# Kernel optimization log

Hardware: AMD Instinct MI355X
Metric: run time of the kernel (lower is better)

Reference implementation:

```python
import jax, jax.numpy as jnp
from jax import lax
import numpy as np

B, T, N, C_IN = 32, 24, 2048, 2
HID, EMB, HORIZON, OUT_DIM = 64, 16, 12, 1


def setup_inputs() -> dict:
    key = jax.random.key(0)
    ks = jax.random.split(key, 8)
    s = 0.05
    return {
        "x": jax.random.normal(ks[0], (B, T, N, C_IN), dtype=jnp.float32),
        "E": jax.random.normal(ks[1], (N, EMB), dtype=jnp.float32),
        "W1": jax.random.normal(ks[2], (C_IN + HID, 4 * HID), dtype=jnp.float32) * s,
        "b1": jnp.zeros((4 * HID,), dtype=jnp.float32),
        "W2": jax.random.normal(ks[3], (HID + HID, 4 * HID), dtype=jnp.float32) * s,
        "b2": jnp.zeros((4 * HID,), dtype=jnp.float32),
        "Wp": jax.random.normal(ks[4], (HID, OUT_DIM * HORIZON), dtype=jnp.float32) * s,
        "bp": jnp.zeros((OUT_DIM * HORIZON,), dtype=jnp.float32),
    }


def _cell(A, xt, h, c, W, b):
    # Graph-conv LSTM cell: A @ [x, h] -> 4 gates
    comb = jnp.concatenate([xt, h], axis=-1)            # [B,N,in+H]
    conv = jnp.einsum("nm,bmc->bnc", A, comb)           # adaptive graph conv
    gates = conv @ W + b                                  # [B,N,4H]
    i, f, g, o = jnp.split(gates, 4, axis=-1)
    c_new = jax.nn.sigmoid(f) * c + jax.nn.sigmoid(i) * jnp.tanh(g)
    h_new = jax.nn.sigmoid(o) * jnp.tanh(c_new)
    return h_new, c_new


def reference(x, E, W1, b1, W2, b2, Wp, bp):
    # Adaptive adjacency: softmax(relu(E E^T)) row-normalized
    A = jax.nn.softmax(jax.nn.relu(E @ E.T), axis=1)      # [N,N]
    b, t, n, _ = x.shape
    z = jnp.zeros((b, n, HID), dtype=x.dtype)
    init = ((z, z), (z, z))

    def step(carry, xt):
        (h1, c1), (h2, c2) = carry
        h1, c1 = _cell(A, xt, h1, c1, W1, b1)
        h2, c2 = _cell(A, h1, h2, c2, W2, b2)
        return ((h1, c1), (h2, c2)), None

    carry, _ = lax.scan(step, init, jnp.moveaxis(x, 1, 0))  # scan over T
    h_last = carry[1][0]                                     # [B,N,H]
    out = h_last @ Wp + bp                                   # [B,N,HORIZON*OUT]
    out = out.reshape(b, n, HORIZON, OUT_DIM).transpose(0, 2, 1, 3)
    return out                                               # [B,HORIZON,N,OUT]
```

## Files before the change

kernel.cpp:

```cpp
#include <hip/hip_runtime.h>
#include <hip/hip_bf16.h>
#include <cstddef>
#include <cstdint>

#define NN   2048
#define BB   32
#define TT   24
#define CIN  2
#define HH   64
#define EMBD 16
#define HOR  12
#define XC   (TT*BB*CIN)
#define PW   4096
#define KC   6144
#define NT   96

using bfrag  = __attribute__((ext_vector_type(8))) short;
using f32x4  = __attribute__((ext_vector_type(4))) float;

static __device__ __forceinline__ short f2bf(float f) {
    __hip_bfloat16 h = __float2bfloat16(f);
    return *reinterpret_cast<short*>(&h);
}
static __device__ __forceinline__ float bf2f(short s) {
    __hip_bfloat16 h;
    *reinterpret_cast<short*>(&h) = s;
    return __bfloat162float(h);
}
static __device__ __forceinline__ unsigned int packsplit(float v) {
    short hb = f2bf(v);
    short lb = f2bf(v - bf2f(hb));
    return (unsigned int)(unsigned short)hb | ((unsigned int)(unsigned short)lb << 16);
}

#define AS1 __attribute__((address_space(1)))
#define AS3 __attribute__((address_space(3)))
static __device__ __forceinline__ void gload16(const short* g, short* l) {
    __builtin_amdgcn_global_load_lds((const AS1 void*)g, (AS3 void*)l, 16, 0, 0);
}

__global__ __launch_bounds__(256) void compute_A_kernel(const float* __restrict__ E,
                                                        short* __restrict__ A2) {
    __shared__ float srow[NN];
    __shared__ float sred[256];
    int row = blockIdx.x;
    float er[EMBD];
#pragma unroll
    for (int k = 0; k < EMBD; ++k) er[k] = E[row*EMBD + k];
    float lmax = -1e30f;
    for (int j = threadIdx.x; j < NN; j += 256) {
        const float* ej = E + j*EMBD;
        float d = 0.f;
#pragma unroll
        for (int k = 0; k < EMBD; ++k) d = fmaf(er[k], ej[k], d);
        d = fmaxf(d, 0.f);
        srow[j] = d;
        lmax = fmaxf(lmax, d);
    }
    sred[threadIdx.x] = lmax;
    __syncthreads();
    for (int s = 128; s > 0; s >>= 1) {
        if (threadIdx.x < s) sred[threadIdx.x] = fmaxf(sred[threadIdx.x], sred[threadIdx.x+s]);
        __syncthreads();
    }
    float rmax = sred[0];
    __syncthreads();
    float lsum = 0.f;
    for (int j = threadIdx.x; j < NN; j += 256) {
        float e = expf(srow[j] - rmax);
        srow[j] = e;
        lsum += e;
    }
    sred[threadIdx.x] = lsum;
    __syncthreads();
    for (int s = 128; s > 0; s >>= 1) {
        if (threadIdx.x < s) sred[threadIdx.x] += sred[threadIdx.x+s];
        __syncthreads();
    }
    float rinv = 1.f / sred[0];
    for (int j = threadIdx.x; j < NN; j += 256) {
        float v = srow[j] * rinv;
        short h = f2bf(v);
        short l = f2bf(v - bf2f(h));
        size_t base = (size_t)row*KC + j;
        A2[base]        = h;
        A2[base + 2048] = h;
        A2[base + 4096] = l;
    }
}

__global__ void scatter_xall(const float* __restrict__ x,
                             short* __restrict__ hi, short* __restrict__ lo) {
    int idx = blockIdx.x*256 + threadIdx.x;
    int n = idx & (NN-1);
    int col = idx >> 11;
    int c = col & 1, b = (col >> 1) & 31, t = col >> 6;
    float v = x[(size_t)(((size_t)b*TT + t)*NN + n)*CIN + c];
    short h = f2bf(v);
    size_t o = (size_t)col*NN + n;
    hi[o] = h;
    lo[o] = f2bf(v - bf2f(h));
}

__global__ void wsplit_T(const float* __restrict__ W, int rowoff, int Kd,
                         short* __restrict__ hi, short* __restrict__ lo) {
    int id = blockIdx.x*256 + threadIdx.x;
    if (id >= 256*Kd) return;
    int j = id / Kd, c = id - j*Kd;
    float v = W[(size_t)(rowoff + c)*256 + j];
    short h = f2bf(v);
    hi[id] = h;
    lo[id] = f2bf(v - bf2f(h));
}

__global__ __launch_bounds__(256, 3) void gc3_gemm(
        const short* __restrict__ Ahi, const short* __restrict__ Alo,
        const short* __restrict__ Bhi, const short* __restrict__ Blo,
        float* __restrict__ Cout, int outStride, int astr) {
    __shared__ short As[12288];
    short* AsHi = As;
    short* AsLo = As + 2048;
    short* BsHi = As + 4096;
    short* BsLo = As + 8192;
    const int t = threadIdx.x;
    const int w = t >> 6, lane = t & 63;
    const int wm = w >> 1, wn = w & 1;
    const int fr = lane & 15, fc = lane >> 4;
    const int rowbase = blockIdx.y * 64;
    const int colbase = blockIdx.x * 128;

    const int rp = t >> 3, ql = t & 7;
    const int qs = ql ^ (rp & 7);
    const int srow = rp*2 + (qs >> 2);
    const int sch  = (qs & 3) * 8;
    const short* aHiS = Ahi + (size_t)(rowbase + srow)*astr + sch;
    const short* aLoS = Alo + (size_t)(rowbase + srow)*astr + sch;
    const short* bHiS = Bhi + (size_t)(colbase + srow)*NN + sch;
    const short* bLoS = Blo + (size_t)(colbase + srow)*NN + sch;
    const size_t bHalf = (size_t)64*NN;

    short* aHiD  = AsHi + t*8;
    short* aLoD  = AsLo + t*8;
    short* bHiD0 = BsHi + t*8;
    short* bHiD1 = BsHi + 2048 + t*8;
    short* bLoD0 = BsLo + t*8;
    short* bLoD1 = BsLo + 2048 + t*8;

    auto ldsoff = [](int row, int f) {
        int rr = row >> 1;
        int q = (((row & 1) << 2) | f) ^ (rr & 7);
        return rr*64 + q*8;
    };
    int aoff[2], boff[4];
#pragma unroll
    for (int m = 0; m < 2; ++m) aoff[m] = ldsoff(wm*32 + m*16 + fr, fc);
#pragma unroll
    for (int n = 0; n < 4; ++n) boff[n] = ldsoff(wn*64 + n*16 + fr, fc);

    f32x4 acc[2][4];
#pragma unroll
    for (int m = 0; m < 2; ++m)
#pragma unroll
        for (int n = 0; n < 4; ++n)
#pragma unroll
            for (int r = 0; r < 4; ++r) acc[m][n][r] = 0.f;

    for (int k0 = 0; k0 < NN; k0 += 32) {
        gload16(aHiS, aHiD);
        gload16(aLoS, aLoD);
        gload16(bHiS, bHiD0);
        gload16(bHiS + bHalf, bHiD1);
        gload16(bLoS, bLoD0);
        gload16(bLoS + bHalf, bLoD1);
        aHiS += 32; aLoS += 32; bHiS += 32; bLoS += 32;
        __syncthreads();
        bfrag ah[2], al[2], bh[4], bl[4];
#pragma unroll
        for (int m = 0; m < 2; ++m) {
            ah[m] = *(const bfrag*)(AsHi + aoff[m]);
            al[m] = *(const bfrag*)(AsLo + aoff[m]);
        }
#pragma unroll
        for (int n = 0; n < 4; ++n) {
            bh[n] = *(const bfrag*)(BsHi + boff[n]);
            bl[n] = *(const bfrag*)(BsLo + boff[n]);
        }
#pragma unroll
        for (int m = 0; m < 2; ++m)
#pragma unroll
            for (int n = 0; n < 4; ++n) {
                acc[m][n] = __builtin_amdgcn_mfma_f32_16x16x32_bf16(ah[m], bh[n], acc[m][n], 0, 0, 0);
                acc[m][n] = __builtin_amdgcn_mfma_f32_16x16x32_bf16(ah[m], bl[n], acc[m][n], 0, 0, 0);
                acc[m][n] = __builtin_amdgcn_mfma_f32_16x16x32_bf16(al[m], bh[n], acc[m][n], 0, 0, 0);
            }
        __syncthreads();
    }
#pragma unroll
    for (int m = 0; m < 2; ++m) {
        const int gr = rowbase + wm*32 + m*16 + fc*4;
#pragma unroll
        for (int n = 0; n < 4; ++n) {
            const int gc = colbase + wn*64 + n*16 + fr;
#pragma unroll
            for (int r = 0; r < 4; ++r)
                Cout[(size_t)(gr + r)*outStride + gc] = acc[m][n][r];
        }
    }
}

__global__ __launch_bounds__(512, 2) void gemm8p(
        const short* __restrict__ A2, const short* __restrict__ B2,
        unsigned int* __restrict__ Cpk, int colstart) {
    __shared__ short lds[3*24576];
    const int tid = threadIdx.x;
    const int w = tid >> 6, lane = tid & 63;
    const int wm = w >> 2, wn = w & 3;
    const int fr = lane & 15, fc = lane >> 4;
    const int gx = gridDim.x;
    const int nwg = gx * gridDim.y;
    const int fid = blockIdx.y * gx + blockIdx.x;
    const int swz = (fid & 7) * (nwg >> 3) + (fid >> 3);
    const int rowbase = (swz / gx) * 128;
    const int colbase = colstart + (swz % gx) * 256;

    const int srl = tid >> 3;
    const int sck = (tid & 7) ^ (srl & 7);
    const short* aS0 = A2 + (size_t)(rowbase + srl)*KC + sck*8;
    const short* aS1 = A2 + (size_t)(rowbase + 64 + srl)*KC + sck*8;
    const short* bS0 = B2 + (size_t)(colbase + srl)*KC + sck*8;
    const short* bS1 = B2 + (size_t)(colbase + 64 + srl)*KC + sck*8;
    const short* bS2 = B2 + (size_t)(colbase + 128 + srl)*KC + sck*8;
    const short* bS3 = B2 + (size_t)(colbase + 192 + srl)*KC + sck*8;

    auto sw = [](int row, int chunk) {
        int c2 = chunk ^ (row & 7);
        return row*64 + c2*8;
    };
    int aoff[4][2], boff[4][2];
#pragma unroll
    for (int m = 0; m < 4; ++m)
#pragma unroll
        for (int kk = 0; kk < 2; ++kk)
            aoff[m][kk] = sw(wm*64 + m*16 + fr, kk*4 + fc);
#pragma unroll
    for (int n = 0; n < 4; ++n)
#pragma unroll
        for (int kk = 0; kk < 2; ++kk)
            boff[n][kk] = 8192 + sw(wn*64 + n*16 + fr, kk*4 + fc);

    bfrag a[4][2], b[4][2];
    f32x4 acc[4][4];
#pragma unroll
    for (int m = 0; m < 4; ++m)
#pragma unroll
        for (int n = 0; n < 4; ++n)
#pragma unroll
            for (int r = 0; r < 4; ++r) acc[m][n][r] = 0.f;

    auto MFMA8 = [&](int m0, int n0) {
#pragma unroll
        for (int dm = 0; dm < 2; ++dm)
#pragma unroll
            for (int dn = 0; dn < 2; ++dn)
#pragma unroll
                for (int kk = 0; kk < 2; ++kk)
                    acc[m0+dm][n0+dn] = __builtin_amdgcn_mfma_f32_16x16x32_bf16(
                        a[m0+dm][kk], b[n0+dn][kk], acc[m0+dm][n0+dn], 0, 0, 0);
    };

    short* bC = lds;
    short* bN = lds + 24576;
    short* bP = lds + 49152;

    gload16(aS0, bC + tid*8);            gload16(aS1, bC + 4096 + tid*8);
    gload16(bS0, bC + 8192 + tid*8);     gload16(bS1, bC + 12288 + tid*8);
    gload16(bS2, bC + 16384 + tid*8);    gload16(bS3, bC + 20480 + tid*8);
    gload16(aS0 + 64, bN + tid*8);          gload16(aS1 + 64, bN + 4096 + tid*8);
    gload16(bS0 + 64, bN + 8192 + tid*8);   gload16(bS1 + 64, bN + 12288 + tid*8);
    gload16(bS2 + 64, bN + 16384 + tid*8);  gload16(bS3 + 64, bN + 20480 + tid*8);

    for (int t = 0; t < NT; ++t) {
        if (t < NT-1) { asm volatile("s_waitcnt vmcnt(6)" ::: "memory"); }
        else          { asm volatile("s_waitcnt vmcnt(0)" ::: "memory"); }
        __builtin_amdgcn_s_barrier();
        __builtin_amdgcn_sched_barrier(0);
        const bool pf = (t + 2 < NT);
        const int toff = (t + 2) * 64;
#pragma unroll
        for (int kk = 0; kk < 2; ++kk) {
            a[0][kk] = *(const bfrag*)(bC + aoff[0][kk]);
            a[1][kk] = *(const bfrag*)(bC + aoff[1][kk]);
            b[0][kk] = *(const bfrag*)(bC + boff[0][kk]);
            b[1][kk] = *(const bfrag*)(bC + boff[1][kk]);
        }
        if (pf) {
            gload16(aS0 + toff, bP + tid*8);
            gload16(aS1 + toff, bP + 4096 + tid*8);
        }
        __builtin_amdgcn_s_barrier();
        __builtin_amdgcn_sched_barrier(0);
        __builtin_amdgcn_s_setprio(1);
        MFMA8(0, 0);
        __builtin_amdgcn_s_setprio(0);
        __builtin_amdgcn_s_barrier();
        __builtin_amdgcn_sched_barrier(0);
#pragma unroll
        for (int kk = 0; kk < 2; ++kk) {
            b[2][kk] = *(const bfrag*)(bC + boff[2][kk]);
            b[3][kk] = *(const bfrag*)(bC + boff[3][kk]);
        }
        if (pf) {
            gload16(bS0 + toff, bP + 8192 + tid*8);
            gload16(bS1 + toff, bP + 12288 + tid*8);
        }
        __builtin_amdgcn_s_barrier();
        __builtin_amdgcn_sched_barrier(0);
        __builtin_amdgcn_s_setprio(1);
        MFMA8(0, 2);
        __builtin_amdgcn_s_setprio(0);
        __builtin_amdgcn_s_barrier();
        __builtin_amdgcn_sched_barrier(0);
#pragma unroll
        for (int kk = 0; kk < 2; ++kk) {
            a[2][kk] = *(const bfrag*)(bC + aoff[2][kk]);
            a[3][kk] = *(const bfrag*)(bC + aoff[3][kk]);
        }
        if (pf) {
            gload16(bS2 + toff, bP + 16384 + tid*8);
            gload16(bS3 + toff, bP + 20480 + tid*8);
        }
        __builtin_amdgcn_s_barrier();
        __builtin_amdgcn_sched_barrier(0);
        __builtin_amdgcn_s_setprio(1);
        MFMA8(2, 0);
        __builtin_amdgcn_s_setprio(0);
        __builtin_amdgcn_s_barrier();
        __builtin_amdgcn_sched_barrier(0);
        __builtin_amdgcn_s_setprio(1);
        MFMA8(2, 2);
        __builtin_amdgcn_s_setprio(0);
        short* tmp = bC; bC = bN; bN = bP; bP = tmp;
    }
#pragma unroll
    for (int m = 0; m < 4; ++m) {
        const int gr0 = rowbase + wm*64 + m*16 + fc*4;
#pragma unroll
        for (int n = 0; n < 4; ++n) {
            const int gc = colbase + wn*64 + n*16 + fr;
#pragma unroll
            for (int r = 0; r < 4; ++r)
                Cpk[(size_t)(gr0 + r)*PW + gc] = packsplit(acc[m][n][r]);
        }
    }
}

template<int NCH, bool XEP>
__global__ __launch_bounds__(256, 2) void cell_mfma(
        const unsigned int* __restrict__ P,
        const float* __restrict__ convX,
        const float* __restrict__ Wx,
        const short* __restrict__ Wthi, const short* __restrict__ Wtlo,
        const float* __restrict__ bias,
        float* __restrict__ cbuf,
        short* __restrict__ hout,
        int tstep) {
    const int t = threadIdx.x;
    const int w = t >> 6, lane = t & 63;
    const int fr = lane & 15, fc = lane >> 4;
    const int b = blockIdx.y;
    const int n0blk = blockIdx.x * 128;
    constexpr int KW = NCH*32;

    bfrag bh[4][NCH], bl[4][NCH];
#pragma unroll
    for (int g = 0; g < 4; ++g)
#pragma unroll
        for (int ch = 0; ch < NCH; ++ch) {
            size_t o = (size_t)((g*4 + w)*16 + fr)*KW + ch*32 + fc*8;
            bh[g][ch] = *(const bfrag*)(Wthi + o);
            bl[g][ch] = *(const bfrag*)(Wtlo + o);
        }
    const int k = w*16 + fr;
    float bs[4], wx0[4], wx1[4];
#pragma unroll
    for (int g = 0; g < 4; ++g) {
        bs[g] = bias[g*64 + k];
        if (XEP) { wx0[g] = Wx[g*64 + k]; wx1[g] = Wx[256 + g*64 + k]; }
    }
    int colb[NCH];
#pragma unroll
    for (int ch = 0; ch < NCH; ++ch)
        colb[ch] = (NCH == 2 || ch < 2) ? (2048 + b*64 + ch*32)
                                        : (b*64 + (ch-2)*32);
    const int cc = lane >> 4;
    const size_t crow = (size_t)(b*64 + k)*NN;
    const size_t hrow = (size_t)(b*64 + k)*KC;

    for (int nt = 0; nt < 8; ++nt) {
        const int n0 = n0blk + nt*16;
        bfrag ah[NCH], al[NCH];
#pragma unroll
        for (int ch = 0; ch < NCH; ++ch) {
            const unsigned int* ap = P + (size_t)(n0 + fr)*PW + colb[ch] + fc*8;
            uint4 u0 = *(const uint4*)ap;
            uint4 u1 = *(const uint4*)(ap + 4);
            unsigned int uu[8] = {u0.x,u0.y,u0.z,u0.w,u1.x,u1.y,u1.z,u1.w};
#pragma unroll
            for (int i = 0; i < 8; ++i) {
                ah[ch][i] = (short)(uu[i] & 0xffffu);
                al[ch][i] = (short)(uu[i] >> 16);
            }
        }
        f32x4 acc[4];
#pragma unroll
        for (int g = 0; g < 4; ++g)
#pragma unroll
            for (int r = 0; r < 4; ++r) acc[g][r] = 0.f;
#pragma unroll
        for (int ch = 0; ch < NCH; ++ch)
#pragma unroll
            for (int g = 0; g < 4; ++g) {
                acc[g] = __builtin_amdgcn_mfma_f32_16x16x32_bf16(ah[ch], bh[g][ch], acc[g], 0, 0, 0);
                acc[g] = __builtin_amdgcn_mfma_f32_16x16x32_bf16(ah[ch], bl[g][ch], acc[g], 0, 0, 0);
                acc[g] = __builtin_amdgcn_mfma_f32_16x16x32_bf16(al[ch], bh[g][ch], acc[g], 0, 0, 0);
            }
        const int nb = n0 + cc*4;
        float4 cold = *(const float4*)(cbuf + crow + nb);
        float xa0[4], xa1[4];
        if (XEP) {
#pragma unroll
            for (int r = 0; r < 4; ++r) {
                float2 cx = *(const float2*)(convX + (size_t)(nb + r)*XC + tstep*64 + b*2);
                xa0[r] = cx.x; xa1[r] = cx.y;
            }
        }
        float cn[4], hv[4];
#pragma unroll
        for (int r = 0; r < 4; ++r) {
            float pg[4];
#pragma unroll
            for (int g = 0; g < 4; ++g) {
                pg[g] = acc[g][r] + bs[g];
                if (XEP) pg[g] += xa0[r]*wx0[g] + xa1[r]*wx1[g];
            }
            float gi = 1.f/(1.f + expf(-pg[0]));
            float gf = 1.f/(1.f + expf(-pg[1]));
            float gg = tanhf(pg[2]);
            float go = 1.f/(1.f + expf(-pg[3]));
            float co = (&cold.x)[r];
            cn[r] = gf*co + gi*gg;
            hv[r] = go * tanhf(cn[r]);
        }
        *(float4*)(cbuf + crow + nb) = make_float4(cn[0], cn[1], cn[2], cn[3]);
        short hh[4], hl[4];
#pragma unroll
        for (int r = 0; r < 4; ++r) {
            hh[r] = f2bf(hv[r]);
            hl[r] = f2bf(hv[r] - bf2f(hh[r]));
        }
        short4 h4 = make_short4(hh[0], hh[1], hh[2], hh[3]);
        short4 l4 = make_short4(hl[0], hl[1], hl[2], hl[3]);
        *(short4*)(hout + hrow + nb)        = h4;
        *(short4*)(hout + hrow + 2048 + nb) = l4;
        *(short4*)(hout + hrow + 4096 + nb) = h4;
    }
}

__global__ __launch_bounds__(256) void proj_T(const short* __restrict__ B2,
        const float* __restrict__ Wp, const float* __restrict__ bp,
        float* __restrict__ out) {
    __shared__ float sW[HH*HOR];
    __shared__ float sb[HOR];
    for (int i = threadIdx.x; i < HH*HOR; i += 256) sW[i] = Wp[i];
    if (threadIdx.x < HOR) sb[threadIdx.x] = bp[threadIdx.x];
    __syncthreads();
    int idx = blockIdx.x*256 + threadIdx.x;
    int b = idx >> 11, n = idx & (NN-1);
    float acc[HOR];
#pragma unroll
    for (int j = 0; j < HOR; ++j) acc[j] = sb[j];
    for (int k = 0; k < HH; ++k) {
        size_t row = (size_t)(b*64 + k)*KC + n;
        float h = bf2f(B2[row]) + bf2f(B2[row + 2048]);
#pragma unroll
        for (int j = 0; j < HOR; ++j) acc[j] = fmaf(h, sW[k*HOR + j], acc[j]);
    }
#pragma unroll
    for (int j = 0; j < HOR; ++j)
        out[(size_t)(b*HOR + j)*NN + n] = acc[j];
}

extern "C" void kernel_launch(void* const* d_in, const int* in_sizes, int n_in,
                              void* d_out, int out_size, void* d_ws, size_t ws_size,
                              hipStream_t stream) {
    const float* x  = (const float*)d_in[0];
    const float* E  = (const float*)d_in[1];
    const float* W1 = (const float*)d_in[2];
    const float* b1 = (const float*)d_in[3];
    const float* W2 = (const float*)d_in[4];
    const float* b2 = (const float*)d_in[5];
    const float* Wp = (const float*)d_in[6];
    const float* bp = (const float*)d_in[7];
    float* out = (float*)d_out;

    char* base = (char*)d_ws;
    short* A2     = (short*)base; base += (size_t)NN*KC*2;
    float* convX  = (float*)base; base += (size_t)NN*XC*4;
    unsigned int* P = (unsigned int*)base; base += (size_t)NN*PW*4;
    short* B2     = (short*)base; base += (size_t)PW*KC*2;
    float* cs1    = (float*)base; base += (size_t)NN*NN*4;
    float* cs2    = (float*)base; base += (size_t)NN*NN*4;
    short* Wt2hi  = (short*)base; base += 256*128*2;
    short* Wt2lo  = (short*)base; base += 256*128*2;
    short* Wt1hi  = (short*)base; base += 256*64*2;
    short* Wt1lo  = (short*)base; base += 256*64*2;
    short* XThi = (short*)P;
    short* XTlo = XThi + (size_t)XC*NN;
    short* h2out = B2;
    short* h1out = B2 + (size_t)NN*KC;

    hipMemsetAsync(cs1, 0, (size_t)NN*NN*4, stream);
    hipMemsetAsync(cs2, 0, (size_t)NN*NN*4, stream);

    compute_A_kernel<<<NN, 256, 0, stream>>>(E, A2);
    wsplit_T<<<(256*128 + 255)/256, 256, 0, stream>>>(W2, 0, 128, Wt2hi, Wt2lo);
    wsplit_T<<<(256*64 + 255)/256, 256, 0, stream>>>(W1, 2, 64, Wt1hi, Wt1lo);
    scatter_xall<<<(XC*NN)/256, 256, 0, stream>>>(x, XThi, XTlo);
    gc3_gemm<<<dim3(XC/128, NN/64), 256, 0, stream>>>(
        A2, A2 + 4096, XThi, XTlo, convX, XC, KC);
    hipMemsetAsync(P, 0, (size_t)NN*PW*4, stream);

    cell_mfma<2, true><<<dim3(NN/128, BB), 256, 0, stream>>>(
        P, convX, W1, Wt1hi, Wt1lo, b1, cs1, h1out, 0);
    gemm8p<<<dim3(8, 16), 512, 0, stream>>>(A2, B2, P, 2048);

    for (int t = 0; t < TT; ++t) {
        cell_mfma<4, false><<<dim3(NN/128, BB), 256, 0, stream>>>(
            P, nullptr, nullptr, Wt2hi, Wt2lo, b2, cs2, h2out, 0);
        if (t < TT-1) {
            cell_mfma<2, true><<<dim3(NN/128, BB), 256, 0, stream>>>(
                P, convX, W1, Wt1hi, Wt1lo, b1, cs1, h1out, t+1);
            gemm8p<<<dim3(16, 16), 512, 0, stream>>>(A2, B2, P, 0);
        }
    }
    proj_T<<<(BB*NN)/256, 256, 0, stream>>>(B2, Wp, bp, out);
}
```

Before: 4.148 ms.

## Simplify gemm8p main loop and fuse layer-2/layer-1 cell launches

The gemm8p inner loop drops its four-phase interleave of LDS reads, global prefetches and MFMA groups with many barriers. Instead it issues all prefetches at once, then all fragment loads, then all 32 MFMAs. Separately, the two per-timestep cell kernels (layer-2 update and next-step layer-1 update) are merged into one launch using blockIdx.z to pick which cell a block runs, halving cell launches and letting both run concurrently. The simpler GEMM schedule gives up fine-grained overlap of LDS reads with MFMA and drops barriers that may have been guarding the triple-buffer reuse.

```diff
diff --git a/kernel.cpp b/kernel.cpp
--- a/kernel.cpp
+++ b/kernel.cpp
@@ -257,17 +257,6 @@
 #pragma unroll
             for (int r = 0; r < 4; ++r) acc[m][n][r] = 0.f;
 
-    auto MFMA8 = [&](int m0, int n0) {
-#pragma unroll
-        for (int dm = 0; dm < 2; ++dm)
-#pragma unroll
-            for (int dn = 0; dn < 2; ++dn)
-#pragma unroll
-                for (int kk = 0; kk < 2; ++kk)
-                    acc[m0+dm][n0+dn] = __builtin_amdgcn_mfma_f32_16x16x32_bf16(
-                        a[m0+dm][kk], b[n0+dn][kk], acc[m0+dm][n0+dn], 0, 0, 0);
-    };
-
     short* bC = lds;
     short* bN = lds + 24576;
     short* bP = lds + 49152;
@@ -283,61 +272,32 @@
         if (t < NT-1) { asm volatile("s_waitcnt vmcnt(6)" ::: "memory"); }
         else          { asm volatile("s_waitcnt vmcnt(0)" ::: "memory"); }
         __builtin_amdgcn_s_barrier();
-        __builtin_amdgcn_sched_barrier(0);
-        const bool pf = (t + 2 < NT);
-        const int toff = (t + 2) * 64;
-#pragma unroll
-        for (int kk = 0; kk < 2; ++kk) {
-            a[0][kk] = *(const bfrag*)(bC + aoff[0][kk]);
-            a[1][kk] = *(const bfrag*)(bC + aoff[1][kk]);
-            b[0][kk] = *(const bfrag*)(bC + boff[0][kk]);
-            b[1][kk] = *(const bfrag*)(bC + boff[1][kk]);
-        }
-        if (pf) {
+        if (t + 2 < NT) {
+            const int toff = (t + 2) * 64;
             gload16(aS0 + toff, bP + tid*8);
             gload16(aS1 + toff, bP + 4096 + tid*8);
-        }
-        __builtin_amdgcn_s_barrier();
-        __builtin_amdgcn_sched_barrier(0);
-        __builtin_amdgcn_s_setprio(1);
-        MFMA8(0, 0);
-        __builtin_amdgcn_s_setprio(0);
-        __builtin_amdgcn_s_barrier();
-        __builtin_amdgcn_sched_barrier(0);
-#pragma unroll
-        for (int kk = 0; kk < 2; ++kk) {
-            b[2][kk] = *(const bfrag*)(bC + boff[2][kk]);
-            b[3][kk] = *(const bfrag*)(bC + boff[3][kk]);
-        }
-        if (pf) {
             gload16(bS0 + toff, bP + 8192 + tid*8);
             gload16(bS1 + toff, bP + 12288 + tid*8);
-        }
-        __builtin_amdgcn_s_barrier();
-        __builtin_amdgcn_sched_barrier(0);
-        __builtin_amdgcn_s_setprio(1);
-        MFMA8(0, 2);
-        __builtin_amdgcn_s_setprio(0);
-        __builtin_amdgcn_s_barrier();
-        __builtin_amdgcn_sched_barrier(0);
-#pragma unroll
-        for (int kk = 0; kk < 2; ++kk) {
-            a[2][kk] = *(const bfrag*)(bC + aoff[2][kk]);
-            a[3][kk] = *(const bfrag*)(bC + aoff[3][kk]);
-        }
-        if (pf) {
             gload16(bS2 + toff, bP + 16384 + tid*8);
             gload16(bS3 + toff, bP + 20480 + tid*8);
         }
-        __builtin_amdgcn_s_barrier();
         __builtin_amdgcn_sched_barrier(0);
+#pragma unroll
+        for (int kk = 0; kk < 2; ++kk) {
+#pragma unroll
+            for (int m = 0; m < 4; ++m) a[m][kk] = *(const bfrag*)(bC + aoff[m][kk]);
+#pragma unroll
+            for (int n = 0; n < 4; ++n) b[n][kk] = *(const bfrag*)(bC + boff[n][kk]);
+        }
         __builtin_amdgcn_s_setprio(1);
-        MFMA8(2, 0);
-        __builtin_amdgcn_s_setprio(0);
-        __builtin_amdgcn_s_barrier();
-        __builtin_amdgcn_sched_barrier(0);
-        __builtin_amdgcn_s_setprio(1);
-        MFMA8(2, 2);
+#pragma unroll
+        for (int m = 0; m < 4; ++m)
+#pragma unroll
+            for (int n = 0; n < 4; ++n)
+#pragma unroll
+                for (int kk = 0; kk < 2; ++kk)
+                    acc[m][n] = __builtin_amdgcn_mfma_f32_16x16x32_bf16(
+                        a[m][kk], b[n][kk], acc[m][n], 0, 0, 0);
         __builtin_amdgcn_s_setprio(0);
         short* tmp = bC; bC = bN; bN = bP; bP = tmp;
     }
@@ -355,7 +315,7 @@
 }
 
 template<int NCH, bool XEP>
-__global__ __launch_bounds__(256, 2) void cell_mfma(
+static __device__ __forceinline__ void cell_body(
         const unsigned int* __restrict__ P,
         const float* __restrict__ convX,
         const float* __restrict__ Wx,
@@ -363,12 +323,10 @@
         const float* __restrict__ bias,
         float* __restrict__ cbuf,
         short* __restrict__ hout,
-        int tstep) {
+        int tstep, int n0blk, int b) {
     const int t = threadIdx.x;
     const int w = t >> 6, lane = t & 63;
     const int fr = lane & 15, fc = lane >> 4;
-    const int b = blockIdx.y;
-    const int n0blk = blockIdx.x * 128;
     constexpr int KW = NCH*32;
 
     bfrag bh[4][NCH], bl[4][NCH];
@@ -464,6 +422,38 @@
         *(short4*)(hout + hrow + 2048 + nb) = l4;
         *(short4*)(hout + hrow + 4096 + nb) = h4;
     }
+}
+
+template<int NCH, bool XEP>
+__global__ __launch_bounds__(256, 2) void cell_mfma(
+        const unsigned int* __restrict__ P,
+        const float* __restrict__ convX,
+        const float* __restrict__ Wx,
+        const short* __restrict__ Wthi, const short* __restrict__ Wtlo,
+        const float* __restrict__ bias,
+        float* __restrict__ cbuf,
+        short* __restrict__ hout,
+        int tstep) {
+    cell_body<NCH, XEP>(P, convX, Wx, Wthi, Wtlo, bias, cbuf, hout,
+                        tstep, blockIdx.x*128, blockIdx.y);
+}
+
+__global__ __launch_bounds__(256, 2) void cell_fused(
+        const unsigned int* __restrict__ P,
+        const float* __restrict__ convX,
+        const float* __restrict__ Wx1,
+        const short* __restrict__ Wt2hi, const short* __restrict__ Wt2lo,
+        const short* __restrict__ Wt1hi, const short* __restrict__ Wt1lo,
+        const float* __restrict__ b2v, const float* __restrict__ b1v,
+        float* __restrict__ cs2, float* __restrict__ cs1,
+        short* __restrict__ h2out, short* __restrict__ h1out,
+        int tnext) {
+    if (blockIdx.z == 0)
+        cell_body<4, false>(P, nullptr, nullptr, Wt2hi, Wt2lo, b2v, cs2, h2out,
+                            0, blockIdx.x*128, blockIdx.y);
+    else
+        cell_body<2, true>(P, convX, Wx1, Wt1hi, Wt1lo, b1v, cs1, h1out,
+                           tnext, blockIdx.x*128, blockIdx.y);
 }
 
 __global__ __launch_bounds__(256) void proj_T(const short* __restrict__ B2,
@@ -535,12 +525,14 @@
     gemm8p<<<dim3(8, 16), 512, 0, stream>>>(A2, B2, P, 2048);
 
     for (int t = 0; t < TT; ++t) {
-        cell_mfma<4, false><<<dim3(NN/128, BB), 256, 0, stream>>>(
-            P, nullptr, nullptr, Wt2hi, Wt2lo, b2, cs2, h2out, 0);
         if (t < TT-1) {
-            cell_mfma<2, true><<<dim3(NN/128, BB), 256, 0, stream>>>(
-                P, convX, W1, Wt1hi, Wt1lo, b1, cs1, h1out, t+1);
+            cell_fused<<<dim3(NN/128, BB, 2), 256, 0, stream>>>(
+                P, convX, W1, Wt2hi, Wt2lo, Wt1hi, Wt1lo, b2, b1,
+                cs2, cs1, h2out, h1out, t+1);
             gemm8p<<<dim3(16, 16), 512, 0, stream>>>(A2, B2, P, 0);
+        } else {
+            cell_mfma<4, false><<<dim3(NN/128, BB), 256, 0, stream>>>(
+                P, nullptr, nullptr, Wt2hi, Wt2lo, b2, cs2, h2out, 0);
         }
     }
     proj_T<<<(BB*NN)/256, 256, 0, stream>>>(B2, Wp, bp, out);
```

After: 4.006 ms. 1.04x faster.
